# Kernel tuning notes

Measured on AMD Instinct MI355X. Metric: run time of the kernel, lower is better.

The kernel has to match this reference:

```python
import jax, jax.numpy as jnp
import numpy as np

EMBED_DIM = 1024
NUM_HEADS = 16
HEAD_DIM = EMBED_DIM // NUM_HEADS
WINDOW = 256


def setup_inputs() -> dict:
    key = jax.random.key(0)
    k1, k2, k3, k4, k5 = jax.random.split(key, 5)
    B, S, E = 4, 4096, EMBED_DIM
    x = jax.random.normal(k1, (B, S, E), dtype=jnp.float32)
    # torch nn.Linear weights: [out_features, in_features]
    s = 1.0 / np.sqrt(E)
    W_qkv = jax.random.uniform(k2, (3 * E, E), dtype=jnp.float32, minval=-s, maxval=s)
    b_qkv = jax.random.uniform(k3, (3 * E,), dtype=jnp.float32, minval=-s, maxval=s)
    W_out = jax.random.uniform(k4, (E, E), dtype=jnp.float32, minval=-s, maxval=s)
    b_out = jax.random.uniform(k5, (E,), dtype=jnp.float32, minval=-s, maxval=s)
    return {"x": x, "W_qkv": W_qkv, "b_qkv": b_qkv, "W_out": W_out, "b_out": b_out}


def reference(x, W_qkv, b_qkv, W_out, b_out):
    B, S, E = x.shape
    H, D, W = NUM_HEADS, HEAD_DIM, WINDOW
    Nw = S // W  # non-overlapping windows; S divisible by W per input specs
    qkv = x @ W_qkv.T + b_qkv                       # [B,S,3E]
    q, k, v = jnp.split(qkv, 3, axis=-1)
    # [B,S,E] -> [B,H,Nw,W,D]
    def to_win(t):
        return t.reshape(B, S, H, D).transpose(0, 2, 1, 3).reshape(B, H, Nw, W, D)
    q, k, v = to_win(q), to_win(k), to_win(v)
    scale = 1.0 / jnp.sqrt(jnp.float32(D))
    scores = jnp.einsum('bhnqd,bhnkd->bhnqk', q, k) * scale
    probs = jax.nn.softmax(scores, axis=-1)
    attn = jnp.einsum('bhnqk,bhnkd->bhnqd', probs, v)  # [B,H,Nw,W,D]
    attn = attn.reshape(B, H, S, D).transpose(0, 2, 1, 3).reshape(B, S, E)
    return attn @ W_out.T + b_out
```

## Files before the change

kernel.cpp:

```cpp
#include <hip/hip_runtime.h>

typedef unsigned short u16;
typedef __bf16 bf16x8 __attribute__((ext_vector_type(8)));
typedef float f32x4 __attribute__((ext_vector_type(4)));
typedef u16 u16x4 __attribute__((ext_vector_type(4)));

#define DEVI static __device__ __forceinline__

DEVI u16 f2bf(float f){
  unsigned u = __float_as_uint(f);
  u += 0x7FFFu + ((u >> 16) & 1u);
  return (u16)(u >> 16);
}

DEVI f32x4 mfma16(bf16x8 a, bf16x8 b, f32x4 c){
  return __builtin_amdgcn_mfma_f32_16x16x32_bf16(a, b, c, 0, 0, 0);
}

DEVI void gld16(u16* lds, const u16* g){
  __builtin_amdgcn_global_load_lds(
      (const __attribute__((address_space(1))) void*)g,
      (__attribute__((address_space(3))) void*)lds, 16, 0, 0);
}

__global__ void cvt_bf16(const float* __restrict__ s, u16* __restrict__ d, int n4){
  int i = blockIdx.x * blockDim.x + threadIdx.x;
  int stride = gridDim.x * blockDim.x;
  for (; i < n4; i += stride){
    float4 v = *(const float4*)(s + (size_t)i * 4);
    u16x4 o = { f2bf(v.x), f2bf(v.y), f2bf(v.z), f2bf(v.w) };
    *(u16x4*)(d + (size_t)i * 4) = o;
  }
}

template<int MODE>
__global__ __launch_bounds__(512, 2)
void gemm_bt(const u16* __restrict__ A, const u16* __restrict__ Bm,
             const float* __restrict__ bias,
             u16* __restrict__ Qws, u16* __restrict__ Kws, u16* __restrict__ Vtws,
             float* __restrict__ Cf)
{
  constexpr int K = 1024;
  constexpr int NT = K / 32;
  __shared__ __align__(16) u16 lds[3 * 16384];
  const int t = threadIdx.x;
  const int w = t >> 6, l = t & 63, g = l >> 4, r16 = l & 15;
  const int wm = w >> 2, wn = w & 3;

  constexpr int NBX = (MODE == 0) ? 12 : 4;
  constexpr int NWG = NBX * 64;
  const int orig = blockIdx.y * NBX + blockIdx.x;
  const int swzb = (orig & 7) * (NWG >> 3) + (orig >> 3);
  const int row0 = (swzb / NBX) * 256, col0 = (swzb % NBX) * 256;

  const f32x4 zero = {0.f, 0.f, 0.f, 0.f};
  f32x4 acc[8][4];
#pragma unroll
  for (int m = 0; m < 8; ++m)
#pragma unroll
    for (int n = 0; n < 4; ++n) acc[m][n] = zero;

  const int F = t >> 3;
  const int cc = (t & 7) ^ (F & 7);
  const int strow = 2 * F + (cc >> 2);
  const int stk = (cc & 3) * 8;
  const u16* pA = A + (size_t)(row0 + strow) * K + stk;
  const u16* pB = Bm + (size_t)(col0 + strow) * K + stk;

  auto STAGE = [&](int buf, int kt){
    u16* dst = lds + buf * 16384 + (w << 9);
    gld16(dst,         pA + kt);
    gld16(dst + 4096,  pA + (size_t)128 * K + kt);
    gld16(dst + 8192,  pB + kt);
    gld16(dst + 12288, pB + (size_t)128 * K + kt);
  };

  const int c1 = (((r16 & 1) << 2) | g) ^ ((r16 >> 1) & 7);
  const int aoff = (wm * 64 + (r16 >> 1)) * 64 + c1 * 8;
  const int boff = 8192 + (wn * 32 + (r16 >> 1)) * 64 + c1 * 8;

  auto TILECOMP = [&](int buf){
    const u16* base = lds + buf * 16384;
    bf16x8 af[8], bfr[4];
#pragma unroll
    for (int m = 0; m < 8; ++m) af[m] = *(const bf16x8*)(base + aoff + m * 512);
#pragma unroll
    for (int n = 0; n < 4; ++n) bfr[n] = *(const bf16x8*)(base + boff + n * 512);
    __builtin_amdgcn_s_setprio(1);
#pragma unroll
    for (int m = 0; m < 8; ++m)
#pragma unroll
      for (int n = 0; n < 4; ++n)
        acc[m][n] = mfma16(af[m], bfr[n], acc[m][n]);
    __builtin_amdgcn_s_setprio(0);
  };

  STAGE(0, 0);
  STAGE(1, 32);
  asm volatile("s_waitcnt vmcnt(4)" ::: "memory");
  __builtin_amdgcn_s_barrier();
  asm volatile("" ::: "memory");

  int cb = 0, sb = 2;
  for (int tt = 0; tt < NT - 2; ++tt){
    STAGE(sb, (tt + 2) * 32);
    TILECOMP(cb);
    asm volatile("s_waitcnt vmcnt(4)" ::: "memory");
    __builtin_amdgcn_s_barrier();
    asm volatile("" ::: "memory");
    cb = (cb == 2) ? 0 : cb + 1;
    sb = (sb == 2) ? 0 : sb + 1;
  }
  TILECOMP(cb);
  cb = (cb == 2) ? 0 : cb + 1;
  asm volatile("s_waitcnt vmcnt(0)" ::: "memory");
  __builtin_amdgcn_s_barrier();
  asm volatile("" ::: "memory");
  TILECOMP(cb);

  float bv[4];
#pragma unroll
  for (int nb = 0; nb < 4; ++nb) bv[nb] = bias[col0 + wn * 64 + nb * 16 + r16];

  if (MODE == 1){
#pragma unroll
    for (int m = 0; m < 8; ++m){
      int row = row0 + wm * 128 + m * 16 + g * 4;
#pragma unroll
      for (int nb = 0; nb < 4; ++nb){
        int n = col0 + wn * 64 + nb * 16 + r16;
#pragma unroll
        for (int j = 0; j < 4; ++j)
          Cf[(size_t)(row + j) * 1024 + n] = acc[m][nb][j] + bv[nb];
      }
    }
  } else {
    const int regn = col0 >> 10;
    if (regn == 0){
#pragma unroll
      for (int m = 0; m < 8; ++m){
        int row = row0 + wm * 128 + m * 16 + g * 4;
#pragma unroll
        for (int nb = 0; nb < 4; ++nb){
          int n = col0 + wn * 64 + nb * 16 + r16;
#pragma unroll
          for (int j = 0; j < 4; ++j)
            Qws[(size_t)(row + j) * 1024 + n] = f2bf(acc[m][nb][j] + bv[nb]);
        }
      }
    } else if (regn == 1){
#pragma unroll
      for (int m = 0; m < 8; ++m){
        int row = row0 + wm * 128 + m * 16 + g * 4;
#pragma unroll
        for (int nb = 0; nb < 4; ++nb){
          int n = col0 + wn * 64 + nb * 16 + r16 - 1024;
#pragma unroll
          for (int j = 0; j < 4; ++j)
            Kws[(size_t)(row + j) * 1024 + n] = f2bf(acc[m][nb][j] + bv[nb]);
        }
      }
    } else {
#pragma unroll
      for (int m = 0; m < 8; ++m){
        int row = row0 + wm * 128 + m * 16 + g * 4;
        int bb = row >> 12, s = row & 4095;
        int wdw = s >> 8, rr = s & 255;
#pragma unroll
        for (int nb = 0; nb < 4; ++nb){
          int n2 = col0 + wn * 64 + nb * 16 + r16 - 2048;
          int hh = n2 >> 6, d = n2 & 63;
          int winw = (bb * 16 + hh) * 16 + wdw;
          u16x4 pk;
#pragma unroll
          for (int j = 0; j < 4; ++j) pk[j] = f2bf(acc[m][nb][j] + bv[nb]);
          *(u16x4*)(Vtws + (size_t)winw * 16384 + d * 256 + rr) = pk;
        }
      }
    }
  }
}

__global__ __launch_bounds__(256, 1)
void attn_win(const u16* __restrict__ Q, const u16* __restrict__ Kws,
              const u16* __restrict__ Vt, u16* __restrict__ Oo)
{
  __shared__ __align__(16) u16 Kl[16384];
  __shared__ __align__(16) u16 Vl[16384];
  __shared__ __align__(16) u16 Pl[16384];
  const int t = threadIdx.x;
  const int wv = t >> 6, l = t & 63, g = l >> 4, r16 = l & 15;
  const int win = blockIdx.x;
  const int b = win >> 8, h = (win >> 4) & 15, wd = win & 15;
  const int s0 = b * 4096 + wd * 256;
  const size_t vwin = (size_t)win * 16384;

  {
    const int rloc = l >> 3, sl = l & 7;
    const u16* ksrc = Kws + (size_t)(s0 + wv * 64 + rloc) * 1024 + h * 64
                      + ((sl ^ rloc) << 3);
#pragma unroll
    for (int j = 0; j < 8; ++j)
      gld16(Kl + wv * 4096 + j * 512, ksrc + (size_t)j * 8 * 1024);
    const int dloc = l >> 5, kcv = (l >> 3) & 3, slv = l & 7;
#pragma unroll
    for (int j = 0; j < 8; ++j){
      int d = wv * 16 + j * 2 + dloc;
      gld16(Vl + (wv * 8 + j) * 512,
            Vt + vwin + (size_t)d * 256 + kcv * 64 + ((slv ^ (d & 7)) << 3));
    }
  }

  bf16x8 aq[4][2];
#pragma unroll
  for (int qm = 0; qm < 4; ++qm)
#pragma unroll
    for (int kk = 0; kk < 2; ++kk)
      aq[qm][kk] = *(const bf16x8*)(Q + (size_t)(s0 + wv * 64 + qm * 16 + r16) * 1024
                                      + h * 64 + kk * 32 + g * 8);

  const f32x4 zero = {0.f, 0.f, 0.f, 0.f};
  f32x4 o[4][4];
  f32x4 lsum[4];
#pragma unroll
  for (int qm = 0; qm < 4; ++qm){
    lsum[qm] = zero;
#pragma unroll
    for (int nd = 0; nd < 4; ++nd) o[qm][nd] = zero;
  }
  bf16x8 onesb;
#pragma unroll
  for (int e = 0; e < 8; ++e) onesb[e] = (__bf16)1.0f;

  const float cl2 = 0.125f * 1.44269504f;

  __syncthreads();

  for (int kc = 0; kc < 4; ++kc){
    f32x4 sc[4][4];
#pragma unroll
    for (int qm = 0; qm < 4; ++qm)
#pragma unroll
      for (int nb = 0; nb < 4; ++nb) sc[qm][nb] = zero;
#pragma unroll
    for (int kk = 0; kk < 2; ++kk){
      bf16x8 kb[4];
#pragma unroll
      for (int nb = 0; nb < 4; ++nb)
        kb[nb] = *(const bf16x8*)(Kl + kc * 4096 + (nb * 16 + r16) * 64
                                  + ((((kk << 2) | g) ^ (r16 & 7)) << 3));
#pragma unroll
      for (int qm = 0; qm < 4; ++qm)
#pragma unroll
        for (int nb = 0; nb < 4; ++nb)
          sc[qm][nb] = mfma16(aq[qm][kk], kb[nb], sc[qm][nb]);
    }

#pragma unroll
    for (int qm = 0; qm < 4; ++qm){
#pragma unroll
      for (int j = 0; j < 4; ++j){
        int q = qm * 16 + g * 4 + j;
        u16* pbase = Pl + wv * 4096 + q * 64;
#pragma unroll
        for (int nb = 0; nb < 4; ++nb){
          float p = __builtin_amdgcn_exp2f(sc[qm][nb][j] * cl2);
          int k = nb * 16 + r16;
          pbase[(k & 7) + (((k >> 3) ^ (q & 7)) << 3)] = f2bf(p);
        }
      }
    }

#pragma unroll
    for (int kc32 = 0; kc32 < 2; ++kc32){
      bf16x8 pa[4], vb[4];
#pragma unroll
      for (int qm = 0; qm < 4; ++qm)
        pa[qm] = *(const bf16x8*)(Pl + wv * 4096 + (qm * 16 + r16) * 64
                                  + ((((kc32 << 2) | g) ^ (r16 & 7)) << 3));
#pragma unroll
      for (int nd = 0; nd < 4; ++nd){
        int d = nd * 16 + r16;
        vb[nd] = *(const bf16x8*)(Vl + d * 256 + kc * 64
                                  + ((((kc32 << 2) | g) ^ (r16 & 7)) << 3));
      }
#pragma unroll
      for (int qm = 0; qm < 4; ++qm){
        lsum[qm] = mfma16(pa[qm], onesb, lsum[qm]);
#pragma unroll
        for (int nd = 0; nd < 4; ++nd)
          o[qm][nd] = mfma16(pa[qm], vb[nd], o[qm][nd]);
      }
    }
  }

#pragma unroll
  for (int qm = 0; qm < 4; ++qm){
#pragma unroll
    for (int j = 0; j < 4; ++j){
      float inv = 1.f / lsum[qm][j];
      int row = s0 + wv * 64 + qm * 16 + g * 4 + j;
#pragma unroll
      for (int nd = 0; nd < 4; ++nd)
        Oo[(size_t)row * 1024 + h * 64 + nd * 16 + r16] = f2bf(o[qm][nd][j] * inv);
    }
  }
}

extern "C" void kernel_launch(void* const* d_in, const int* in_sizes, int n_in,
                              void* d_out, int out_size, void* d_ws, size_t ws_size,
                              hipStream_t stream)
{
  (void)in_sizes; (void)n_in; (void)out_size; (void)ws_size;
  const float* x  = (const float*)d_in[0];
  const float* Wq = (const float*)d_in[1];
  const float* bq = (const float*)d_in[2];
  const float* Wo = (const float*)d_in[3];
  const float* bo = (const float*)d_in[4];

  char* ws = (char*)d_ws;
  const size_t SZ = (size_t)16384 * 1024 * 2;
  u16* xb  = (u16*)(ws);
  u16* Vt  = (u16*)(ws + SZ);
  u16* wqb = (u16*)(ws + 2 * SZ);
  u16* wob = (u16*)(ws + 2 * SZ + 6291456);
  u16* Qws = (u16*)d_out;
  u16* Kws = (u16*)d_out + (size_t)16384 * 1024;

  cvt_bf16<<<2048, 256, 0, stream>>>(x,  xb,  16777216 / 4);
  cvt_bf16<<<768,  256, 0, stream>>>(Wq, wqb, 3145728 / 4);
  cvt_bf16<<<256,  256, 0, stream>>>(Wo, wob, 1048576 / 4);

  gemm_bt<0><<<dim3(12, 64), 512, 0, stream>>>(xb, wqb, bq, Qws, Kws, Vt, nullptr);

  attn_win<<<1024, 256, 0, stream>>>(Qws, Kws, Vt, xb);

  gemm_bt<1><<<dim3(4, 64), 512, 0, stream>>>(xb, wob, bo,
                                              nullptr, nullptr, nullptr,
                                              (float*)d_out);
}
```

Baseline: 217.8 us.

## Split QKV GEMM tile compute into two interleaved halves with staged loads

For the MODE 0 (QKV projection) GEMM, each k-tile's work is split into two halves of 4x4 MFMAs. A and B global-to-LDS loads are issued between the halves, and extra barriers and lgkmcnt waits are added so fragment reads, async loads and MFMA bursts interleave across waves in a ping-pong schedule. This is meant to cut register pressure (fewer live A fragments) and overlap memory issue with matrix compute. The cost is more barriers per tile and the risk of stalls if waves desynchronize.

```diff
diff --git a/kernel.cpp b/kernel.cpp
--- a/kernel.cpp
+++ b/kernel.cpp
@@ -67,6 +67,10 @@
   const u16* pA = A + (size_t)(row0 + strow) * K + stk;
   const u16* pB = Bm + (size_t)(col0 + strow) * K + stk;
 
+  const int c1 = (((r16 & 1) << 2) | g) ^ ((r16 >> 1) & 7);
+  const int aoff = (wm * 64 + (r16 >> 1)) * 64 + c1 * 8;
+  const int boff = 8192 + (wn * 32 + (r16 >> 1)) * 64 + c1 * 8;
+
   auto STAGE = [&](int buf, int kt){
     u16* dst = lds + buf * 16384 + (w << 9);
     gld16(dst,         pA + kt);
@@ -75,48 +79,106 @@
     gld16(dst + 12288, pB + (size_t)128 * K + kt);
   };
 
-  const int c1 = (((r16 & 1) << 2) | g) ^ ((r16 >> 1) & 7);
-  const int aoff = (wm * 64 + (r16 >> 1)) * 64 + c1 * 8;
-  const int boff = 8192 + (wn * 32 + (r16 >> 1)) * 64 + c1 * 8;
-
-  auto TILECOMP = [&](int buf){
-    const u16* base = lds + buf * 16384;
-    bf16x8 af[8], bfr[4];
-#pragma unroll
-    for (int m = 0; m < 8; ++m) af[m] = *(const bf16x8*)(base + aoff + m * 512);
-#pragma unroll
-    for (int n = 0; n < 4; ++n) bfr[n] = *(const bf16x8*)(base + boff + n * 512);
-    __builtin_amdgcn_s_setprio(1);
-#pragma unroll
-    for (int m = 0; m < 8; ++m)
-#pragma unroll
-      for (int n = 0; n < 4; ++n)
-        acc[m][n] = mfma16(af[m], bfr[n], acc[m][n]);
-    __builtin_amdgcn_s_setprio(0);
-  };
-
-  STAGE(0, 0);
-  STAGE(1, 32);
-  asm volatile("s_waitcnt vmcnt(4)" ::: "memory");
-  __builtin_amdgcn_s_barrier();
-  asm volatile("" ::: "memory");
-
-  int cb = 0, sb = 2;
-  for (int tt = 0; tt < NT - 2; ++tt){
-    STAGE(sb, (tt + 2) * 32);
-    TILECOMP(cb);
+  if (MODE == 0){
+    auto TILE = [&](int cb, int sb, int kt2, int smode){
+      const u16* base = lds + cb * 16384;
+      u16* sdst = lds + sb * 16384 + (w << 9);
+      bf16x8 aX[4], bX[4];
+#pragma unroll
+      for (int m = 0; m < 4; ++m) aX[m] = *(const bf16x8*)(base + aoff + m * 512);
+#pragma unroll
+      for (int n = 0; n < 4; ++n) bX[n] = *(const bf16x8*)(base + boff + n * 512);
+      if (smode == 2){
+        gld16(sdst,        pA + kt2);
+        gld16(sdst + 4096, pA + (size_t)128 * K + kt2);
+      }
+      __builtin_amdgcn_s_barrier();
+      asm volatile("s_waitcnt lgkmcnt(0)" ::: "memory");
+      __builtin_amdgcn_s_setprio(1);
+#pragma unroll
+      for (int m = 0; m < 4; ++m)
+#pragma unroll
+        for (int n = 0; n < 4; ++n)
+          acc[m][n] = mfma16(aX[m], bX[n], acc[m][n]);
+      __builtin_amdgcn_s_setprio(0);
+      __builtin_amdgcn_s_barrier();
+      bf16x8 aY[4];
+#pragma unroll
+      for (int m = 0; m < 4; ++m) aY[m] = *(const bf16x8*)(base + aoff + (m + 4) * 512);
+      if (smode == 2){
+        gld16(sdst + 8192,  pB + kt2);
+        gld16(sdst + 12288, pB + (size_t)128 * K + kt2);
+      }
+      __builtin_amdgcn_s_barrier();
+      asm volatile("s_waitcnt lgkmcnt(0)" ::: "memory");
+      __builtin_amdgcn_s_setprio(1);
+#pragma unroll
+      for (int m = 0; m < 4; ++m)
+#pragma unroll
+        for (int n = 0; n < 4; ++n)
+          acc[m + 4][n] = mfma16(aY[m], bX[n], acc[m + 4][n]);
+      __builtin_amdgcn_s_setprio(0);
+      if (smode == 2)      asm volatile("s_waitcnt vmcnt(4)" ::: "memory");
+      else if (smode == 1) asm volatile("s_waitcnt vmcnt(0)" ::: "memory");
+      __builtin_amdgcn_s_barrier();
+      asm volatile("" ::: "memory");
+    };
+
+    STAGE(0, 0);
+    STAGE(1, 32);
     asm volatile("s_waitcnt vmcnt(4)" ::: "memory");
     __builtin_amdgcn_s_barrier();
     asm volatile("" ::: "memory");
+
+    int cb = 0, sb = 2;
+    for (int tt = 0; tt < NT - 2; ++tt){
+      TILE(cb, sb, (tt + 2) * 32, 2);
+      cb = (cb == 2) ? 0 : cb + 1;
+      sb = (sb == 2) ? 0 : sb + 1;
+    }
+    TILE(cb, sb, 0, 1);
     cb = (cb == 2) ? 0 : cb + 1;
-    sb = (sb == 2) ? 0 : sb + 1;
-  }
-  TILECOMP(cb);
-  cb = (cb == 2) ? 0 : cb + 1;
-  asm volatile("s_waitcnt vmcnt(0)" ::: "memory");
-  __builtin_amdgcn_s_barrier();
-  asm volatile("" ::: "memory");
-  TILECOMP(cb);
+    TILE(cb, sb, 0, 0);
+  } else {
+    auto TILECOMP = [&](int buf){
+      const u16* base = lds + buf * 16384;
+      bf16x8 af[8], bfr[4];
+#pragma unroll
+      for (int m = 0; m < 8; ++m) af[m] = *(const bf16x8*)(base + aoff + m * 512);
+#pragma unroll
+      for (int n = 0; n < 4; ++n) bfr[n] = *(const bf16x8*)(base + boff + n * 512);
+      __builtin_amdgcn_s_setprio(1);
+#pragma unroll
+      for (int m = 0; m < 8; ++m)
+#pragma unroll
+        for (int n = 0; n < 4; ++n)
+          acc[m][n] = mfma16(af[m], bfr[n], acc[m][n]);
+      __builtin_amdgcn_s_setprio(0);
+    };
+
+    STAGE(0, 0);
+    STAGE(1, 32);
+    asm volatile("s_waitcnt vmcnt(4)" ::: "memory");
+    __builtin_amdgcn_s_barrier();
+    asm volatile("" ::: "memory");
+
+    int cb = 0, sb = 2;
+    for (int tt = 0; tt < NT - 2; ++tt){
+      STAGE(sb, (tt + 2) * 32);
+      TILECOMP(cb);
+      asm volatile("s_waitcnt vmcnt(4)" ::: "memory");
+      __builtin_amdgcn_s_barrier();
+      asm volatile("" ::: "memory");
+      cb = (cb == 2) ? 0 : cb + 1;
+      sb = (sb == 2) ? 0 : sb + 1;
+    }
+    TILECOMP(cb);
+    cb = (cb == 2) ? 0 : cb + 1;
+    asm volatile("s_waitcnt vmcnt(0)" ::: "memory");
+    __builtin_amdgcn_s_barrier();
+    asm volatile("" ::: "memory");
+    TILECOMP(cb);
+  }
 
   float bv[4];
 #pragma unroll
```

Result: no change. 221.8 us (+1.8%).

## Restructure GEMM main loop into BK=64 tiles with 4-phase interleaved staging

Applied to the files above, without the earlier changes.

The GEMM k-tile grows from 32 to 64, and the triple-buffered LDS is replaced by a double-buffered scheme of 64KB per stage. Each tile is split into four phases that interleave LDS fragment reads, async global-to-LDS loads for the next A and B sub-tiles, and MFMA bursts, with barriers between phases. The goal is to halve the number of outer iterations and to overlap memory traffic with compute at a finer grain. In exchange there are more barriers per tile, a larger LDS footprint (128KB per block) that may limit occupancy at 2 blocks per CU, and a complex B-ahead prefetch ordering that must stay correct.

```diff
diff --git a/kernel.cpp b/kernel.cpp
--- a/kernel.cpp
+++ b/kernel.cpp
@@ -41,8 +41,8 @@
              float* __restrict__ Cf)
 {
   constexpr int K = 1024;
-  constexpr int NT = K / 32;
-  __shared__ __align__(16) u16 lds[3 * 16384];
+  constexpr int NT = K / 64;
+  __shared__ __align__(16) u16 lds[2 * 32768];
   const int t = threadIdx.x;
   const int w = t >> 6, l = t & 63, g = l >> 4, r16 = l & 15;
   const int wm = w >> 2, wn = w & 3;
@@ -60,63 +60,88 @@
 #pragma unroll
     for (int n = 0; n < 4; ++n) acc[m][n] = zero;
 
-  const int F = t >> 3;
-  const int cc = (t & 7) ^ (F & 7);
-  const int strow = 2 * F + (cc >> 2);
-  const int stk = (cc & 3) * 8;
-  const u16* pA = A + (size_t)(row0 + strow) * K + stk;
-  const u16* pB = Bm + (size_t)(col0 + strow) * K + stk;
-
-  auto STAGE = [&](int buf, int kt){
-    u16* dst = lds + buf * 16384 + (w << 9);
-    gld16(dst,         pA + kt);
-    gld16(dst + 4096,  pA + (size_t)128 * K + kt);
-    gld16(dst + 8192,  pB + kt);
-    gld16(dst + 12288, pB + (size_t)128 * K + kt);
+  const int trow = t >> 3;
+  const int tcol = (t & 7) ^ (trow & 7);
+  const u16* pA = A + (size_t)(row0 + trow) * K + tcol * 8;
+  const u16* pB = Bm + (size_t)(col0 + trow) * K + tcol * 8;
+
+  const int sk0 = ((g) ^ (r16 & 7)) << 3;
+  const int sk1 = ((4 | g) ^ (r16 & 7)) << 3;
+  const int aoffb = (wm * 128 + r16) * 64;
+  const int boffb = 16384 + (wn * 64 + r16) * 64;
+
+  bf16x8 bfr[4][2];
+
+  auto PHASE = [&](const u16* base, int mq, u16* sdst, const u16* ssrc,
+                   int endvm){
+    bf16x8 a0[2], a1[2];
+    if (mq == 0){
+#pragma unroll
+      for (int n = 0; n < 4; ++n){
+        bfr[n][0] = *(const bf16x8*)(base + boffb + n * 1024 + sk0);
+        bfr[n][1] = *(const bf16x8*)(base + boffb + n * 1024 + sk1);
+      }
+    }
+    a0[0] = *(const bf16x8*)(base + aoffb + (2 * mq) * 1024 + sk0);
+    a0[1] = *(const bf16x8*)(base + aoffb + (2 * mq) * 1024 + sk1);
+    a1[0] = *(const bf16x8*)(base + aoffb + (2 * mq + 1) * 1024 + sk0);
+    a1[1] = *(const bf16x8*)(base + aoffb + (2 * mq + 1) * 1024 + sk1);
+    if (sdst){
+      gld16(sdst,        ssrc);
+      gld16(sdst + 4096, ssrc + (size_t)64 * K);
+    }
+    __builtin_amdgcn_s_barrier();
+    asm volatile("s_waitcnt lgkmcnt(0)" ::: "memory");
+    __builtin_amdgcn_sched_barrier(0);
+    __builtin_amdgcn_s_setprio(1);
+#pragma unroll
+    for (int n = 0; n < 4; ++n){
+      acc[2 * mq][n]     = mfma16(a0[0], bfr[n][0], acc[2 * mq][n]);
+      acc[2 * mq][n]     = mfma16(a0[1], bfr[n][1], acc[2 * mq][n]);
+      acc[2 * mq + 1][n] = mfma16(a1[0], bfr[n][0], acc[2 * mq + 1][n]);
+      acc[2 * mq + 1][n] = mfma16(a1[1], bfr[n][1], acc[2 * mq + 1][n]);
+    }
+    __builtin_amdgcn_s_setprio(0);
+    if (endvm == 4)      asm volatile("s_waitcnt vmcnt(4)" ::: "memory");
+    else if (endvm == 0) asm volatile("s_waitcnt vmcnt(0)" ::: "memory");
+    __builtin_amdgcn_s_barrier();
+    asm volatile("" ::: "memory");
   };
 
-  const int c1 = (((r16 & 1) << 2) | g) ^ ((r16 >> 1) & 7);
-  const int aoff = (wm * 64 + (r16 >> 1)) * 64 + c1 * 8;
-  const int boff = 8192 + (wn * 32 + (r16 >> 1)) * 64 + c1 * 8;
-
-  auto TILECOMP = [&](int buf){
-    const u16* base = lds + buf * 16384;
-    bf16x8 af[8], bfr[4];
-#pragma unroll
-    for (int m = 0; m < 8; ++m) af[m] = *(const bf16x8*)(base + aoff + m * 512);
-#pragma unroll
-    for (int n = 0; n < 4; ++n) bfr[n] = *(const bf16x8*)(base + boff + n * 512);
-    __builtin_amdgcn_s_setprio(1);
-#pragma unroll
-    for (int m = 0; m < 8; ++m)
-#pragma unroll
-      for (int n = 0; n < 4; ++n)
-        acc[m][n] = mfma16(af[m], bfr[n], acc[m][n]);
-    __builtin_amdgcn_s_setprio(0);
+  auto TILE = [&](int p, int kA, int kB, int endvm){
+    const u16* base = lds + p * 32768;
+    u16* aw = lds + (p ^ 1) * 32768 + (w << 9);
+    u16* bw = lds + p * 32768 + 16384 + (w << 9);
+    PHASE(base, 0, kA >= 0 ? aw        : nullptr, pA + kA, -1);
+    PHASE(base, 1, kA >= 0 ? aw + 8192 : nullptr, pA + (size_t)128 * K + kA, -1);
+    PHASE(base, 2, kB >= 0 ? bw        : nullptr, pB + kB, -1);
+    PHASE(base, 3, kB >= 0 ? bw + 8192 : nullptr, pB + (size_t)128 * K + kB, endvm);
   };
 
-  STAGE(0, 0);
-  STAGE(1, 32);
+  {
+    u16* d0 = lds + (w << 9);
+    gld16(d0,                 pA);
+    gld16(d0 + 4096,          pA + (size_t)64 * K);
+    gld16(d0 + 8192,          pA + (size_t)128 * K);
+    gld16(d0 + 12288,         pA + (size_t)192 * K);
+    gld16(d0 + 16384,         pB);
+    gld16(d0 + 16384 + 4096,  pB + (size_t)64 * K);
+    gld16(d0 + 16384 + 8192,  pB + (size_t)128 * K);
+    gld16(d0 + 16384 + 12288, pB + (size_t)192 * K);
+    u16* d1 = lds + 32768 + 16384 + (w << 9);
+    gld16(d1,         pB + 64);
+    gld16(d1 + 4096,  pB + (size_t)64 * K + 64);
+    gld16(d1 + 8192,  pB + (size_t)128 * K + 64);
+    gld16(d1 + 12288, pB + (size_t)192 * K + 64);
+  }
   asm volatile("s_waitcnt vmcnt(4)" ::: "memory");
   __builtin_amdgcn_s_barrier();
   asm volatile("" ::: "memory");
 
-  int cb = 0, sb = 2;
-  for (int tt = 0; tt < NT - 2; ++tt){
-    STAGE(sb, (tt + 2) * 32);
-    TILECOMP(cb);
-    asm volatile("s_waitcnt vmcnt(4)" ::: "memory");
-    __builtin_amdgcn_s_barrier();
-    asm volatile("" ::: "memory");
-    cb = (cb == 2) ? 0 : cb + 1;
-    sb = (sb == 2) ? 0 : sb + 1;
-  }
-  TILECOMP(cb);
-  cb = (cb == 2) ? 0 : cb + 1;
-  asm volatile("s_waitcnt vmcnt(0)" ::: "memory");
-  __builtin_amdgcn_s_barrier();
-  asm volatile("" ::: "memory");
-  TILECOMP(cb);
+  for (int tt = 0; tt < NT - 2; ++tt)
+    TILE(tt & 1, (tt + 1) * 64, (tt + 2) * 64, 4);
+  TILE(0, (NT - 1) * 64, -1, 0);
+  TILE(1, -1, -1, -1);
 
   float bv[4];
 #pragma unroll
```

Result: slower. 230.7 us (+5.9%).
